# Performance work log

Hardware: AMD Instinct MI355X
Metric: run time of the kernel (lower is better)

Reference implementation:

```python
import jax, jax.numpy as jnp
import numpy as np

N_MB = 4  # number of micro-behavior buckets; C = N_MB**2 + 1

def setup_inputs() -> dict:
    key = jax.random.key(0)
    k_q, k_k, k_b, k_w, k_a = jax.random.split(key, 5)
    b, h, S, d = 8, 8, 512, 64
    C = N_MB * N_MB + 1
    return {
        "query": jax.random.normal(k_q, (b, h, S, d), dtype=jnp.float32),
        "key": jax.random.normal(k_k, (b, h, S, d), dtype=jnp.float32),
        "b_seq": jax.random.randint(k_b, (b, S), 0, N_MB + 1, dtype=jnp.int32),
        "W1": jax.random.normal(k_w, (N_MB, h, d, d), dtype=jnp.float32) * 0.02,
        "alpha1": jax.random.normal(k_a, (C, N_MB, h), dtype=jnp.float32) * 0.02,
    }

def reference(query, key, b_seq, W1, alpha1):
    # bucket-pair index per (i, j) token pair; 0 if either token is padding
    bi = b_seq[:, :, None]  # [b, S, 1]
    bj = b_seq[:, None, :]  # [b, 1, S]
    b_mat = ((bi - 1) * N_MB + bj) * (bi * bj != 0).astype(jnp.int32)  # [b, S, S]
    # mix the n_mb base bilinear weights into C per-bucket-pair matrices
    W1_ = jnp.einsum('Bhmn,CBh->Chmn', W1, jax.nn.softmax(alpha1, axis=1))
    # full bilinear score for every bucket-pair class C (the wasteful part)
    att_all = jnp.einsum('bhim,Chmn,bhjn->bhijC', query, W1_, key)  # [b,h,S,S,C]
    # select the score matching each pair's bucket index
    idx = b_mat[:, None, :, :, None].astype(jnp.int32)  # [b,1,S,S,1] -> broadcast over h
    idx = jnp.broadcast_to(idx, att_all.shape[:4] + (1,))
    scores = jnp.take_along_axis(att_all, idx, axis=4)[..., 0]  # [b,h,S,S]
    return scores
```

## Files before the change

### kernel.cpp

```cpp
#include <hip/hip_runtime.h>
#include <stdint.h>

#define NB 4
#define NC 17
#define HH 8
#define SS 512
#define DD 64

typedef __attribute__((ext_vector_type(8))) short bf16x8;
typedef __attribute__((ext_vector_type(4))) float f32x4;

#define WS_W1   0
#define WS_T    1114112
#define WS_RIDX (WS_T + 20971520)
#define WS_GST  (WS_RIDX + 16384)

__device__ __forceinline__ unsigned short f2bf(float f) {
  unsigned int x; __builtin_memcpy(&x, &f, 4);
  return (unsigned short)((x + 0x7fff + ((x >> 16) & 1)) >> 16);
}
__device__ __forceinline__ bf16x8 cvt8(const float* p) {
  float4 a = *(const float4*)p;
  float4 b = *(const float4*)(p + 4);
  union { bf16x8 v; unsigned short u[8]; } t;
  t.u[0] = f2bf(a.x); t.u[1] = f2bf(a.y); t.u[2] = f2bf(a.z); t.u[3] = f2bf(a.w);
  t.u[4] = f2bf(b.x); t.u[5] = f2bf(b.y); t.u[6] = f2bf(b.z); t.u[7] = f2bf(b.w);
  return t.v;
}

__global__ __launch_bounds__(256) void k_prep(const int* __restrict__ bseq,
                                              const float* __restrict__ W1,
                                              const float* __restrict__ alpha,
                                              int* __restrict__ ridx,
                                              int* __restrict__ gst,
                                              unsigned short* __restrict__ W1mbf) {
  int tid = threadIdx.x;
  if (blockIdx.x < 8) {
    int b = blockIdx.x;
    __shared__ int cnt[5], base[6], cur[5];
    if (tid < 5) cnt[tid] = 0;
    __syncthreads();
    for (int j = tid; j < SS; j += blockDim.x) atomicAdd(&cnt[bseq[b * SS + j]], 1);
    __syncthreads();
    if (tid == 0) {
      base[0] = 0;
      for (int k = 0; k < 5; k++) base[k + 1] = base[k] + cnt[k];
      for (int k = 0; k < 6; k++) gst[b * 6 + k] = base[k];
    }
    __syncthreads();
    if (tid < 5) cur[tid] = base[tid];
    __syncthreads();
    for (int j = tid; j < SS; j += blockDim.x) {
      int p = atomicAdd(&cur[bseq[b * SS + j]], 1);
      ridx[b * SS + p] = j;
    }
  } else {
    int cb = blockIdx.x - 8;
    int c = cb >> 3, hh = cb & 7;
    __shared__ float sm[NB];
    if (tid == 0) {
      float a[NB], mx = -1e30f;
      for (int B = 0; B < NB; B++) { a[B] = alpha[(c * NB + B) * HH + hh]; mx = fmaxf(mx, a[B]); }
      float s = 0.f;
      for (int B = 0; B < NB; B++) { a[B] = __expf(a[B] - mx); s += a[B]; }
      for (int B = 0; B < NB; B++) sm[B] = a[B] / s;
    }
    __syncthreads();
    float s0 = sm[0], s1 = sm[1], s2 = sm[2], s3 = sm[3];
    for (int idx = tid; idx < DD * DD; idx += blockDim.x) {
      float v = W1[((0 * HH + hh) * DD * DD) + idx] * s0 +
                W1[((1 * HH + hh) * DD * DD) + idx] * s1 +
                W1[((2 * HH + hh) * DD * DD) + idx] * s2 +
                W1[((3 * HH + hh) * DD * DD) + idx] * s3;
      W1mbf[((size_t)(c * HH + hh)) * DD * DD + idx] = f2bf(v);
    }
  }
}

__global__ __launch_bounds__(256) void k_T(const float* __restrict__ key,
                                           const unsigned short* __restrict__ W1mbf,
                                           const int* __restrict__ ridx,
                                           const int* __restrict__ gst,
                                           unsigned short* __restrict__ Tg) {
  int bx = blockIdx.x;
  int half = bx & 1, t = bx >> 1;
  int B = t % 5, bh = t / 5, b = bh >> 3, h = bh & 7;
  int tid = threadIdx.x, wave = tid >> 6, lane = tid & 63;
  int quad = lane >> 4, l16 = lane & 15;
  int slot = wave + 4 * half;
  int flat = 0;
  for (int a = 0; a < 5; a++) {
    int gs = gst[b * 6 + a], ge = gst[b * 6 + a + 1];
    int c = (B == 0 || a == 0) ? 0 : (B - 1) * NB + a;
    const unsigned short* Wc = W1mbf + (size_t)(c * HH + h) * DD * DD;
    for (int p0 = gs; p0 < ge; p0 += 16, flat++) {
      if ((flat & 7) != slot) continue;
      int p = p0 + l16; if (p > ge - 1) p = ge - 1;
      int j = ridx[b * SS + p];
      const float* kp = &key[((size_t)(bh * SS + j)) * DD + quad * 8];
      bf16x8 af0 = cvt8(kp);
      bf16x8 af1 = cvt8(kp + 32);
      f32x4 accs[4];
#pragma unroll
      for (int nt = 0; nt < 4; nt++) {
        const unsigned short* wp = &Wc[(nt * 16 + l16) * DD + quad * 8];
        bf16x8 b0 = *(const bf16x8*)wp;
        bf16x8 b1 = *(const bf16x8*)(wp + 32);
        f32x4 acc = {0.f, 0.f, 0.f, 0.f};
        acc = __builtin_amdgcn_mfma_f32_16x16x32_bf16(af0, b0, acc, 0, 0, 0);
        acc = __builtin_amdgcn_mfma_f32_16x16x32_bf16(af1, b1, acc, 0, 0, 0);
        accs[nt] = acc;
      }
      int jr[4];
#pragma unroll
      for (int reg = 0; reg < 4; reg++) {
        int pr = p0 + quad * 4 + reg;
        jr[reg] = (pr < ge) ? ridx[b * SS + pr] : -1;
      }
#pragma unroll
      for (int nt = 0; nt < 4; nt++)
#pragma unroll
        for (int reg = 0; reg < 4; reg++)
          if (jr[reg] >= 0)
            Tg[((size_t)((bh * 5 + B) * SS + jr[reg])) * DD + nt * 16 + l16] =
                f2bf(accs[nt][reg]);
    }
  }
}

__global__ __launch_bounds__(256) void k_scores(const float* __restrict__ query,
                                                const unsigned short* __restrict__ Tg,
                                                const int* __restrict__ ridx,
                                                const int* __restrict__ gst,
                                                float* __restrict__ out) {
  int bx = blockIdx.x;
  int jq = bx & 3, t = bx >> 2;
  int B = t % 5, bh = t / 5, b = bh >> 3;
  int tid = threadIdx.x, wave = tid >> 6, lane = tid & 63;
  int quad = lane >> 4, l16 = lane & 15;
  int gs = gst[b * 6 + B], ge = gst[b * 6 + B + 1];
  int n = ge - gs;
  if (n <= 0) return;
  const unsigned short* Tp = Tg + (size_t)(bh * 5 + B) * SS * DD;
  for (int mt = wave; mt * 16 < n; mt += 4) {
    int p0 = gs + mt * 16;
    int p = p0 + l16; if (p > ge - 1) p = ge - 1;
    int r = ridx[b * SS + p];
    const float* qp = &query[((size_t)(bh * SS + r)) * DD + quad * 8];
    bf16x8 af0 = cvt8(qp);
    bf16x8 af1 = cvt8(qp + 32);
    int rr[4];
#pragma unroll
    for (int reg = 0; reg < 4; reg++) {
      int pr = p0 + quad * 4 + reg;
      rr[reg] = (pr < ge) ? ridx[b * SS + pr] : -1;
    }
#pragma unroll
    for (int nt8 = 0; nt8 < 8; nt8++) {
      int j0 = (jq * 8 + nt8) * 16;
      const unsigned short* tp = &Tp[(size_t)(j0 + l16) * DD + quad * 8];
      bf16x8 b0 = *(const bf16x8*)tp;
      bf16x8 b1 = *(const bf16x8*)(tp + 32);
      f32x4 acc = {0.f, 0.f, 0.f, 0.f};
      acc = __builtin_amdgcn_mfma_f32_16x16x32_bf16(af0, b0, acc, 0, 0, 0);
      acc = __builtin_amdgcn_mfma_f32_16x16x32_bf16(af1, b1, acc, 0, 0, 0);
#pragma unroll
      for (int reg = 0; reg < 4; reg++)
        if (rr[reg] >= 0)
          out[((size_t)(bh * SS + rr[reg])) * SS + j0 + l16] = acc[reg];
    }
  }
}

extern "C" void kernel_launch(void* const* d_in, const int* in_sizes, int n_in,
                              void* d_out, int out_size, void* d_ws, size_t ws_size,
                              hipStream_t stream) {
  const float* q = (const float*)d_in[0];
  const float* k = (const float*)d_in[1];
  const int* bseq = (const int*)d_in[2];
  const float* W1 = (const float*)d_in[3];
  const float* alpha = (const float*)d_in[4];
  float* out = (float*)d_out;
  char* ws = (char*)d_ws;
  unsigned short* W1mbf = (unsigned short*)(ws + WS_W1);
  unsigned short* Tg = (unsigned short*)(ws + WS_T);
  int* ridx = (int*)(ws + WS_RIDX);
  int* gst = (int*)(ws + WS_GST);

  hipLaunchKernelGGL(k_prep, dim3(8 + NC * HH), dim3(256), 0, stream,
                     bseq, W1, alpha, ridx, gst, W1mbf);
  hipLaunchKernelGGL(k_T, dim3(64 * 5 * 2), dim3(256), 0, stream,
                     k, W1mbf, ridx, gst, Tg);
  hipLaunchKernelGGL(k_scores, dim3(64 * 5 * 4), dim3(256), 0, stream,
                     q, Tg, ridx, gst, out);
}
```

Before: 139.5 us.

## Fuse key-transform and score kernels with per-tile transformed keys in LDS

Merges the T = key·W1_c kernel and the scores kernel into one kernel. Each block owns a 128-column slice of keys, builds the five per-query-bucket transformed key tiles in shared memory, then computes scores for all query rows against that slice. This removes the 20 MB global round trip for T and one launch. In exchange the grid shrinks to 256 blocks of 512 threads with about 92 KB of LDS each, and every block re-reads all query rows.

```diff
diff --git a/kernel.cpp b/kernel.cpp
--- a/kernel.cpp
+++ b/kernel.cpp
@@ -11,8 +11,7 @@
 typedef __attribute__((ext_vector_type(4))) float f32x4;
 
 #define WS_W1   0
-#define WS_T    1114112
-#define WS_RIDX (WS_T + 20971520)
+#define WS_RIDX 1114112
 #define WS_GST  (WS_RIDX + 16384)
 
 __device__ __forceinline__ unsigned short f2bf(float f) {
@@ -77,97 +76,114 @@
   }
 }
 
-__global__ __launch_bounds__(256) void k_T(const float* __restrict__ key,
-                                           const unsigned short* __restrict__ W1mbf,
-                                           const int* __restrict__ ridx,
-                                           const int* __restrict__ gst,
-                                           unsigned short* __restrict__ Tg) {
+__global__ __launch_bounds__(512) void k_fused(const float* __restrict__ query,
+                                               const float* __restrict__ key,
+                                               const int* __restrict__ bseq,
+                                               const unsigned short* __restrict__ W1mbf,
+                                               const int* __restrict__ ridx,
+                                               const int* __restrict__ gst,
+                                               float* __restrict__ out) {
   int bx = blockIdx.x;
-  int half = bx & 1, t = bx >> 1;
-  int B = t % 5, bh = t / 5, b = bh >> 3, h = bh & 7;
+  int jt = bx & 3, bh = bx >> 2, b = bh >> 3, h = bh & 7;
+  int j0 = jt * 128;
   int tid = threadIdx.x, wave = tid >> 6, lane = tid & 63;
   int quad = lane >> 4, l16 = lane & 15;
-  int slot = wave + 4 * half;
+
+  __shared__ __align__(16) unsigned short Tl[5][128][72];
+  __shared__ int ord[128], lgs[6], cnt[5], cur[5];
+
+  if (tid < 5) cnt[tid] = 0;
+  __syncthreads();
+  int mybj = 0;
+  if (tid < 128) { mybj = bseq[b * SS + j0 + tid]; atomicAdd(&cnt[mybj], 1); }
+  __syncthreads();
+  if (tid == 0) {
+    lgs[0] = 0;
+    for (int a = 0; a < 5; a++) lgs[a + 1] = lgs[a] + cnt[a];
+  }
+  __syncthreads();
+  if (tid < 5) cur[tid] = lgs[tid];
+  __syncthreads();
+  if (tid < 128) ord[atomicAdd(&cur[mybj], 1)] = tid;
+  __syncthreads();
+
   int flat = 0;
   for (int a = 0; a < 5; a++) {
-    int gs = gst[b * 6 + a], ge = gst[b * 6 + a + 1];
-    int c = (B == 0 || a == 0) ? 0 : (B - 1) * NB + a;
-    const unsigned short* Wc = W1mbf + (size_t)(c * HH + h) * DD * DD;
+    int ls = lgs[a], le = lgs[a + 1];
+    if (le <= ls) continue;
+    int nB = (a == 0) ? 1 : 5;
+    for (int B = 0; B < nB; B++) {
+      int c = (B == 0) ? 0 : (B - 1) * NB + a;
+      const unsigned short* Wc = W1mbf + (size_t)(c * HH + h) * DD * DD;
+      for (int t0 = ls; t0 < le; t0 += 16, flat++) {
+        if ((flat & 7) != wave) continue;
+        int p = t0 + l16; if (p > le - 1) p = le - 1;
+        int cl = ord[p];
+        const float* kp = &key[((size_t)(bh * SS + j0 + cl)) * DD + quad * 8];
+        bf16x8 af0 = cvt8(kp);
+        bf16x8 af1 = cvt8(kp + 32);
+        int cr[4];
+#pragma unroll
+        for (int reg = 0; reg < 4; reg++) {
+          int pr = t0 + quad * 4 + reg;
+          cr[reg] = (pr < le) ? ord[pr] : -1;
+        }
+#pragma unroll
+        for (int nt = 0; nt < 4; nt++) {
+          const unsigned short* wp = &Wc[(nt * 16 + l16) * DD + quad * 8];
+          bf16x8 b0 = *(const bf16x8*)wp;
+          bf16x8 b1 = *(const bf16x8*)(wp + 32);
+          f32x4 acc = {0.f, 0.f, 0.f, 0.f};
+          acc = __builtin_amdgcn_mfma_f32_16x16x32_bf16(af0, b0, acc, 0, 0, 0);
+          acc = __builtin_amdgcn_mfma_f32_16x16x32_bf16(af1, b1, acc, 0, 0, 0);
+#pragma unroll
+          for (int reg = 0; reg < 4; reg++) {
+            if (cr[reg] >= 0) {
+              unsigned short v = f2bf(acc[reg]);
+              if (a == 0) {
+#pragma unroll
+                for (int Bw = 0; Bw < 5; Bw++) Tl[Bw][cr[reg]][nt * 16 + l16] = v;
+              } else {
+                Tl[B][cr[reg]][nt * 16 + l16] = v;
+              }
+            }
+          }
+        }
+      }
+    }
+  }
+  __syncthreads();
+
+  flat = 0;
+  for (int B = 0; B < 5; B++) {
+    int gs = gst[b * 6 + B], ge = gst[b * 6 + B + 1];
+    if (ge <= gs) continue;
     for (int p0 = gs; p0 < ge; p0 += 16, flat++) {
-      if ((flat & 7) != slot) continue;
+      if ((flat & 7) != wave) continue;
       int p = p0 + l16; if (p > ge - 1) p = ge - 1;
-      int j = ridx[b * SS + p];
-      const float* kp = &key[((size_t)(bh * SS + j)) * DD + quad * 8];
-      bf16x8 af0 = cvt8(kp);
-      bf16x8 af1 = cvt8(kp + 32);
-      f32x4 accs[4];
-#pragma unroll
-      for (int nt = 0; nt < 4; nt++) {
-        const unsigned short* wp = &Wc[(nt * 16 + l16) * DD + quad * 8];
-        bf16x8 b0 = *(const bf16x8*)wp;
-        bf16x8 b1 = *(const bf16x8*)(wp + 32);
+      int r = ridx[b * SS + p];
+      const float* qp = &query[((size_t)(bh * SS + r)) * DD + quad * 8];
+      bf16x8 af0 = cvt8(qp);
+      bf16x8 af1 = cvt8(qp + 32);
+      int rr[4];
+#pragma unroll
+      for (int reg = 0; reg < 4; reg++) {
+        int pr = p0 + quad * 4 + reg;
+        rr[reg] = (pr < ge) ? ridx[b * SS + pr] : -1;
+      }
+#pragma unroll
+      for (int ct = 0; ct < 8; ct++) {
+        const unsigned short* tp = &Tl[B][ct * 16 + l16][quad * 8];
+        bf16x8 b0 = *(const bf16x8*)tp;
+        bf16x8 b1 = *(const bf16x8*)(tp + 32);
         f32x4 acc = {0.f, 0.f, 0.f, 0.f};
         acc = __builtin_amdgcn_mfma_f32_16x16x32_bf16(af0, b0, acc, 0, 0, 0);
         acc = __builtin_amdgcn_mfma_f32_16x16x32_bf16(af1, b1, acc, 0, 0, 0);
-        accs[nt] = acc;
+#pragma unroll
+        for (int reg = 0; reg < 4; reg++)
+          if (rr[reg] >= 0)
+            out[((size_t)(bh * SS + rr[reg])) * SS + j0 + ct * 16 + l16] = acc[reg];
       }
-      int jr[4];
-#pragma unroll
-      for (int reg = 0; reg < 4; reg++) {
-        int pr = p0 + quad * 4 + reg;
-        jr[reg] = (pr < ge) ? ridx[b * SS + pr] : -1;
-      }
-#pragma unroll
-      for (int nt = 0; nt < 4; nt++)
-#pragma unroll
-        for (int reg = 0; reg < 4; reg++)
-          if (jr[reg] >= 0)
-            Tg[((size_t)((bh * 5 + B) * SS + jr[reg])) * DD + nt * 16 + l16] =
-                f2bf(accs[nt][reg]);
-    }
-  }
-}
-
-__global__ __launch_bounds__(256) void k_scores(const float* __restrict__ query,
-                                                const unsigned short* __restrict__ Tg,
-                                                const int* __restrict__ ridx,
-                                                const int* __restrict__ gst,
-                                                float* __restrict__ out) {
-  int bx = blockIdx.x;
-  int jq = bx & 3, t = bx >> 2;
-  int B = t % 5, bh = t / 5, b = bh >> 3;
-  int tid = threadIdx.x, wave = tid >> 6, lane = tid & 63;
-  int quad = lane >> 4, l16 = lane & 15;
-  int gs = gst[b * 6 + B], ge = gst[b * 6 + B + 1];
-  int n = ge - gs;
-  if (n <= 0) return;
-  const unsigned short* Tp = Tg + (size_t)(bh * 5 + B) * SS * DD;
-  for (int mt = wave; mt * 16 < n; mt += 4) {
-    int p0 = gs + mt * 16;
-    int p = p0 + l16; if (p > ge - 1) p = ge - 1;
-    int r = ridx[b * SS + p];
-    const float* qp = &query[((size_t)(bh * SS + r)) * DD + quad * 8];
-    bf16x8 af0 = cvt8(qp);
-    bf16x8 af1 = cvt8(qp + 32);
-    int rr[4];
-#pragma unroll
-    for (int reg = 0; reg < 4; reg++) {
-      int pr = p0 + quad * 4 + reg;
-      rr[reg] = (pr < ge) ? ridx[b * SS + pr] : -1;
-    }
-#pragma unroll
-    for (int nt8 = 0; nt8 < 8; nt8++) {
-      int j0 = (jq * 8 + nt8) * 16;
-      const unsigned short* tp = &Tp[(size_t)(j0 + l16) * DD + quad * 8];
-      bf16x8 b0 = *(const bf16x8*)tp;
-      bf16x8 b1 = *(const bf16x8*)(tp + 32);
-      f32x4 acc = {0.f, 0.f, 0.f, 0.f};
-      acc = __builtin_amdgcn_mfma_f32_16x16x32_bf16(af0, b0, acc, 0, 0, 0);
-      acc = __builtin_amdgcn_mfma_f32_16x16x32_bf16(af1, b1, acc, 0, 0, 0);
-#pragma unroll
-      for (int reg = 0; reg < 4; reg++)
-        if (rr[reg] >= 0)
-          out[((size_t)(bh * SS + rr[reg])) * SS + j0 + l16] = acc[reg];
     }
   }
 }
@@ -183,14 +199,11 @@
   float* out = (float*)d_out;
   char* ws = (char*)d_ws;
   unsigned short* W1mbf = (unsigned short*)(ws + WS_W1);
-  unsigned short* Tg = (unsigned short*)(ws + WS_T);
   int* ridx = (int*)(ws + WS_RIDX);
   int* gst = (int*)(ws + WS_GST);
 
   hipLaunchKernelGGL(k_prep, dim3(8 + NC * HH), dim3(256), 0, stream,
                      bseq, W1, alpha, ridx, gst, W1mbf);
-  hipLaunchKernelGGL(k_T, dim3(64 * 5 * 2), dim3(256), 0, stream,
-                     k, W1mbf, ridx, gst, Tg);
-  hipLaunchKernelGGL(k_scores, dim3(64 * 5 * 4), dim3(256), 0, stream,
-                     q, Tg, ridx, gst, out);
-}
+  hipLaunchKernelGGL(k_fused, dim3(64 * 4), dim3(512), 0, stream,
+                     q, k, bseq, W1mbf, ridx, gst, out);
+}
```

After: 124.2 us. -10.9%, faster.
